# Kernel tuning notes

Measured on AMD Instinct MI355X. Metric: run time of the kernel, lower is better.

## Reference

```python
import jax, jax.numpy as jnp
import numpy as np

N, E_FULL, E_G = 20000, 640000, 160000
IN_DIM, OUT_DIM, H, EDGE_DIM = 128, 16, 8, 128
HD = OUT_DIM * H
SCALE = float(np.sqrt(OUT_DIM))


def setup_inputs() -> dict:
    key = jax.random.key(0)
    ks = jax.random.split(key, 16)

    def lin(k, fi, fo):
        return jax.random.normal(k, (fi, fo), jnp.float32) / np.float32(np.sqrt(fi))

    return {
        "h": jax.random.normal(ks[0], (N, IN_DIM), jnp.float32),
        "e": jax.random.normal(ks[1], (E_G, EDGE_DIM), jnp.float32),
        "adj2": jax.random.uniform(ks[2], (E_FULL, 1), jnp.float32),
        "rel_pos_3d": jax.random.normal(ks[3], (E_FULL, 1), jnp.float32),
        "src": jax.random.randint(ks[4], (E_FULL,), 0, N),
        "dst": jax.random.randint(ks[5], (E_FULL,), 0, N),
        "edge_map": jnp.arange(E_G),  # g's edges are a (unique) subset of full_g's edges
        "Wq": lin(ks[6], IN_DIM, HD), "bq": jnp.zeros((HD,), jnp.float32),
        "Wk": lin(ks[7], IN_DIM, HD), "bk": jnp.zeros((HD,), jnp.float32),
        "Wv": lin(ks[8], IN_DIM, HD), "bv": jnp.zeros((HD,), jnp.float32),
        "Wpe": lin(ks[9], EDGE_DIM, H), "bpe": jnp.zeros((H,), jnp.float32),
        "Wap": lin(ks[10], H, EDGE_DIM), "bap": jnp.zeros((EDGE_DIM,), jnp.float32),
        "Wout": lin(ks[11], HD, HD), "bout": jnp.zeros((HD,), jnp.float32),
        "Woute": lin(ks[12], EDGE_DIM, EDGE_DIM), "boute": jnp.zeros((EDGE_DIM,), jnp.float32),
    }


def reference(h, e, adj2, rel_pos_3d, src, dst, edge_map,
              Wq, bq, Wk, bk, Wv, bv, Wpe, bpe, Wap, bap,
              Wout, bout, Woute, boute):
    Qh = (h @ Wq + bq).reshape(N, H, OUT_DIM)
    Kh = (h @ Wk + bk).reshape(N, H, OUT_DIM)
    Vh = (h @ Wv + bv).reshape(N, H, OUT_DIM)
    proj_e = e @ Wpe + bpe                                       # [E_g, H]

    # full_g edge pipeline: src_dot_dst -> scaling -> dot_exp
    dot = jnp.einsum('ehd,ehd->eh', Kh[src], Qh[dst]) / SCALE    # [E_full, H]
    score = jnp.exp(jnp.clip(dot, -5.0, 5.0) * adj2) + rel_pos_3d  # [E_full, H]

    # extract g's scores, fuse edge features, scatter back
    g_score = score[edge_map]                                    # [E_g, H]
    e_out = g_score @ Wap + bap                                  # attn_proj, [E_g, edge_dim]
    g_score = jnp.clip(g_score, -5.0, 5.0) + proj_e              # imp_exp_attn
    score = score.at[edge_map].set(g_score)                      # partUpdataScore
    score = jnp.exp(jnp.clip(score, -5.0, 5.0))                  # exp

    # send_and_recv: weighted-sum aggregation over full_g edges
    wV = jax.ops.segment_sum(Vh[src] * score[:, :, None], dst, num_segments=N)  # [N, H, D]
    z = jax.ops.segment_sum(score, dst, num_segments=N)                          # [N, H]

    h_out = (wV / (z[:, :, None] + 1e-6)).reshape(N, HD) @ Wout + bout
    e_out = (e_out + e) @ Woute + boute
    return h_out, e_out
```

## Files before the change

kernel.cpp:

```cpp
#include <hip/hip_runtime.h>
#include <hip/hip_bf16.h>

#define NN 20000
#define EF 640000
#define EG 160000
#define SCAN_B 79

typedef __attribute__((ext_vector_type(8))) short bf16x8;
typedef __attribute__((ext_vector_type(4))) float f32x4;
typedef __attribute__((ext_vector_type(2))) float f32x2;

__device__ inline short f2bf(float f) {
    union { float f; unsigned u; } x; x.f = f;
    unsigned r = x.u + 0x7FFF + ((x.u >> 16) & 1);
    return (short)(r >> 16);
}
__device__ inline float bf2f(short s) {
    union { float f; unsigned u; } x;
    x.u = ((unsigned)(unsigned short)s) << 16;
    return x.f;
}
__device__ inline float blo(unsigned u) {
    union { float f; unsigned u; } c; c.u = u << 16; return c.f;
}
__device__ inline float bhi(unsigned u) {
    union { float f; unsigned u; } c; c.u = u & 0xFFFF0000u; return c.f;
}
__device__ inline unsigned pk2(float a, float b) {
    return (unsigned)(unsigned short)f2bf(a) | ((unsigned)(unsigned short)f2bf(b) << 16);
}
__device__ inline float clip5(float v) { return fminf(fmaxf(v, -5.f), 5.f); }

__global__ __launch_bounds__(256) void prep_kernel(
    int* __restrict__ hist, int* __restrict__ inv,
    const float* __restrict__ W0, const float* __restrict__ W1,
    const float* __restrict__ W2, const float* __restrict__ W3,
    const float* __restrict__ W4, short* __restrict__ B0,
    short* __restrict__ B1, short* __restrict__ B2,
    short* __restrict__ B3, short* __restrict__ B4,
    const float* __restrict__ Wpe, short* __restrict__ WpeF,
    const float* __restrict__ Wap, const float* __restrict__ bap,
    const float* __restrict__ Woute, const float* __restrict__ boute,
    short* __restrict__ WcombF, float* __restrict__ bcomb)
{
    int b = blockIdx.x;
    int tid = threadIdx.x;
    if (b < 2500) {
        int i = b * 256 + tid;
        if (i < NN) hist[i] = 0;
        if (i < EF) inv[i] = -1;
    } else if (b < 2540) {
        int u = b - 2500;
        int mat = u >> 3, blk = u & 7;
        const float* W; short* B;
        switch (mat) {
            case 0: W = W0; B = B0; break;
            case 1: W = W1; B = B1; break;
            case 2: W = W2; B = B2; break;
            case 3: W = W3; B = B3; break;
            default: W = W4; B = B4; break;
        }
        int i = blk * 256 + tid;
        int f = i >> 6, lane = i & 63;
        int n = f >> 2, ks = f & 3;
        int col = n * 16 + (lane & 15);
        int k0 = ks * 32 + (lane >> 4) * 8;
        #pragma unroll
        for (int j = 0; j < 8; ++j)
            B[(size_t)i * 8 + j] = f2bf(W[(size_t)(k0 + j) * 128 + col]);
    } else if (b == 2540) {
        int i = tid;
        int lane = i & 63;
        int ks = i >> 6;
        int l15 = lane & 15, lhi = lane >> 4;
        #pragma unroll
        for (int j = 0; j < 8; ++j) {
            int k = ks * 32 + lhi * 8 + j;
            WpeF[(size_t)i * 8 + j] = (l15 < 8) ? f2bf(Wpe[k * 8 + l15]) : 0;
        }
    } else {
        int j = tid;
        if (j < 128) {
            #pragma unroll
            for (int t = 0; t < 32; ++t) WcombF[j * 32 + t] = 0;
        }
        __syncthreads();
        if (j < 128) {
            float bc = boute[j];
            for (int k = 0; k < 128; ++k) bc += bap[k] * Woute[k * 128 + j];
            bcomb[j] = bc;
            int n = j >> 4, l15 = j & 15;
            #pragma unroll
            for (int i = 0; i < 8; ++i) {
                float s = 0.f;
                for (int k = 0; k < 128; ++k) s += Wap[i * 128 + k] * Woute[k * 128 + j];
                WcombF[((size_t)n * 64 + l15) * 8 + i] = f2bf(s);
            }
        }
    }
}

__global__ __launch_bounds__(256) void histinv_kernel(
    const int* __restrict__ dst, int* __restrict__ hist,
    const int* __restrict__ emap, int* __restrict__ inv)
{
    int i = blockIdx.x * 256 + threadIdx.x;
    if (i < EF) atomicAdd(&hist[dst[i]], 1);
    if (i < EG) inv[emap[i]] = i;
}

__global__ __launch_bounds__(256, 2) void qkv_fused(
    const float* __restrict__ h,
    const short* __restrict__ WqF, const short* __restrict__ WkF,
    const short* __restrict__ WvF,
    const float* __restrict__ bq, const float* __restrict__ bk,
    const float* __restrict__ bv,
    short* __restrict__ Qb, short* __restrict__ Kb,
    unsigned char* __restrict__ K8, unsigned char* __restrict__ V8)
{
    int lane = threadIdx.x & 63;
    int w = threadIdx.x >> 6;
    int l15 = lane & 15, lhi = lane >> 4;

    #pragma unroll
    for (int sel = 0; sel < 3; ++sel) {
        const short* BF  = sel == 0 ? WqF : sel == 1 ? WkF : WvF;
        const float* bias = sel == 0 ? bq : sel == 1 ? bk : bv;
        bf16x8 bf[8][4];
        #pragma unroll
        for (int n = 0; n < 8; ++n)
            #pragma unroll
            for (int ks = 0; ks < 4; ++ks)
                bf[n][ks] = *(const bf16x8*)(BF + ((size_t)((n * 4 + ks) * 64 + lane)) * 8);

        for (int t = blockIdx.x; t < 313; t += gridDim.x) {
            int r = t * 64 + w * 16 + l15;
            bool ok = r < NN;
            bf16x8 a[4];
            #pragma unroll
            for (int ks = 0; ks < 4; ++ks) {
                if (ok) {
                    const float* ap = h + (size_t)r * 128 + ks * 32 + lhi * 8;
                    float4 f0 = *(const float4*)ap;
                    float4 f1 = *(const float4*)(ap + 4);
                    a[ks][0] = f2bf(f0.x); a[ks][1] = f2bf(f0.y);
                    a[ks][2] = f2bf(f0.z); a[ks][3] = f2bf(f0.w);
                    a[ks][4] = f2bf(f1.x); a[ks][5] = f2bf(f1.y);
                    a[ks][6] = f2bf(f1.z); a[ks][7] = f2bf(f1.w);
                } else {
                    #pragma unroll
                    for (int j = 0; j < 8; ++j) a[ks][j] = 0;
                }
            }
            #pragma unroll
            for (int n = 0; n < 8; ++n) {
                f32x4 acc = (f32x4){0.f, 0.f, 0.f, 0.f};
                #pragma unroll
                for (int ks = 0; ks < 4; ++ks)
                    acc = __builtin_amdgcn_mfma_f32_16x16x32_bf16(bf[n][ks], a[ks], acc, 0, 0, 0);
                if (!ok) continue;
                int col0 = n * 16 + lhi * 4;
                float4 bs = *(const float4*)(bias + col0);
                float g0 = acc[0] + bs.x, g1 = acc[1] + bs.y;
                float g2 = acc[2] + bs.z, g3 = acc[3] + bs.w;
                if (sel == 0) {
                    *(uint2*)(Qb + (size_t)r * 128 + col0) =
                        make_uint2(pk2(g0, g1), pk2(g2, g3));
                } else if (sel == 1) {
                    *(uint2*)(Kb + (size_t)r * 128 + col0) =
                        make_uint2(pk2(g0, g1), pk2(g2, g3));
                    int w8 = __builtin_amdgcn_cvt_pk_fp8_f32(g0, g1, 0, false);
                    w8 = __builtin_amdgcn_cvt_pk_fp8_f32(g2, g3, w8, true);
                    *(unsigned*)(K8 + (size_t)r * 128 + col0) = (unsigned)w8;
                } else {
                    int w8 = __builtin_amdgcn_cvt_pk_fp8_f32(g0, g1, 0, false);
                    w8 = __builtin_amdgcn_cvt_pk_fp8_f32(g2, g3, w8, true);
                    *(unsigned*)(V8 + (size_t)r * 128 + col0) = (unsigned)w8;
                }
            }
        }
    }
}

__global__ __launch_bounds__(256, 2) void mfma_gemm_abf16(
    const short* __restrict__ Ap, const short* __restrict__ BF,
    const float* __restrict__ bias, float* __restrict__ out, int M)
{
    int lane = threadIdx.x & 63;
    int w = threadIdx.x >> 6;
    int l15 = lane & 15, lhi = lane >> 4;

    bf16x8 bf[8][4];
    #pragma unroll
    for (int n = 0; n < 8; ++n)
        #pragma unroll
        for (int ks = 0; ks < 4; ++ks)
            bf[n][ks] = *(const bf16x8*)(BF + ((size_t)((n * 4 + ks) * 64 + lane)) * 8);

    int ntile = (M + 63) / 64;
    for (int t = blockIdx.x; t < ntile; t += gridDim.x) {
        int r = t * 64 + w * 16 + l15;
        bool ok = r < M;
        bf16x8 a[4];
        #pragma unroll
        for (int ks = 0; ks < 4; ++ks) {
            if (ok) a[ks] = *(const bf16x8*)(Ap + (size_t)r * 128 + ks * 32 + lhi * 8);
            else {
                #pragma unroll
                for (int j = 0; j < 8; ++j) a[ks][j] = 0;
            }
        }
        #pragma unroll
        for (int n = 0; n < 8; ++n) {
            f32x4 acc = (f32x4){0.f, 0.f, 0.f, 0.f};
            #pragma unroll
            for (int ks = 0; ks < 4; ++ks)
                acc = __builtin_amdgcn_mfma_f32_16x16x32_bf16(bf[n][ks], a[ks], acc, 0, 0, 0);
            if (!ok) continue;
            int col0 = n * 16 + lhi * 4;
            float4 bs = *(const float4*)(bias + col0);
            *(float4*)(out + (size_t)r * 128 + col0) =
                make_float4(acc[0] + bs.x, acc[1] + bs.y, acc[2] + bs.z, acc[3] + bs.w);
        }
    }
}

__global__ __launch_bounds__(256) void score_g_kernel(
    const short* __restrict__ Qb, const short* __restrict__ Kb,
    const int* __restrict__ src, const int* __restrict__ dst,
    const float* __restrict__ adj2, const float* __restrict__ rel,
    const int* __restrict__ emap,
    short* __restrict__ gsb, float* __restrict__ s1f)
{
    int tid = blockIdx.x * 256 + threadIdx.x;
    if (tid >= EG * 8) return;
    int i = tid >> 3, hh = tid & 7;
    int e = emap[i];
    int s = src[e], d = dst[e];
    const bf16x8* Kp = (const bf16x8*)(Kb + (size_t)s * 128 + hh * 16);
    const bf16x8* Qp = (const bf16x8*)(Qb + (size_t)d * 128 + hh * 16);
    bf16x8 k0 = Kp[0], k1 = Kp[1];
    bf16x8 q0 = Qp[0], q1 = Qp[1];
    float dot = 0.f;
    #pragma unroll
    for (int j = 0; j < 8; ++j) dot += bf2f(k0[j]) * bf2f(q0[j]);
    #pragma unroll
    for (int j = 0; j < 8; ++j) dot += bf2f(k1[j]) * bf2f(q1[j]);
    dot *= 0.25f;
    float s1 = __expf(clip5(dot) * adj2[e]) + rel[e];
    gsb[tid] = f2bf(s1);
    s1f[tid] = s1;
}

__global__ __launch_bounds__(256, 3) void mfma_eout_pe(
    const float* __restrict__ Ap, const short* __restrict__ WouteF,
    const short* __restrict__ WcombF, const float* __restrict__ bcomb,
    const short* __restrict__ gsb, const short* __restrict__ WpeF,
    const float* __restrict__ bpe, const float* __restrict__ s1f,
    float* __restrict__ out, float* __restrict__ scoreg)
{
    __shared__ short ldsW[16384];
    int tid = threadIdx.x;
    #pragma unroll
    for (int i = 0; i < 8; ++i)
        ((uint4*)ldsW)[tid + i * 256] = ((const uint4*)WouteF)[tid + i * 256];

    int lane = tid & 63;
    int w = tid >> 6;
    int l15 = lane & 15, lhi = lane >> 4;
    int r = blockIdx.x * 64 + w * 16 + l15;

    bf16x8 bc8[8], bp[4];
    #pragma unroll
    for (int n = 0; n < 8; ++n)
        bc8[n] = *(const bf16x8*)(WcombF + ((size_t)(n * 64 + lane)) * 8);
    #pragma unroll
    for (int ks = 0; ks < 4; ++ks)
        bp[ks] = *(const bf16x8*)(WpeF + ((size_t)(ks * 64 + lane)) * 8);

    bf16x8 a[4], ag;
    #pragma unroll
    for (int ks = 0; ks < 4; ++ks) {
        const float* ap = Ap + (size_t)r * 128 + ks * 32 + lhi * 8;
        float4 f0 = *(const float4*)ap;
        float4 f1 = *(const float4*)(ap + 4);
        a[ks][0] = f2bf(f0.x); a[ks][1] = f2bf(f0.y);
        a[ks][2] = f2bf(f0.z); a[ks][3] = f2bf(f0.w);
        a[ks][4] = f2bf(f1.x); a[ks][5] = f2bf(f1.y);
        a[ks][6] = f2bf(f1.z); a[ks][7] = f2bf(f1.w);
    }
    if (lhi == 0) ag = *(const bf16x8*)(gsb + (size_t)r * 8);
    else {
        #pragma unroll
        for (int j = 0; j < 8; ++j) ag[j] = 0;
    }
    __syncthreads();

    #pragma unroll
    for (int n = 0; n < 8; ++n) {
        f32x4 acc = (f32x4){0.f, 0.f, 0.f, 0.f};
        #pragma unroll
        for (int ks = 0; ks < 4; ++ks) {
            bf16x8 b = *(const bf16x8*)(ldsW + ((n * 4 + ks) * 64 + lane) * 8);
            acc = __builtin_amdgcn_mfma_f32_16x16x32_bf16(b, a[ks], acc, 0, 0, 0);
        }
        acc = __builtin_amdgcn_mfma_f32_16x16x32_bf16(bc8[n], ag, acc, 0, 0, 0);
        int col0 = n * 16 + lhi * 4;
        float4 bs = *(const float4*)(bcomb + col0);
        *(float4*)(out + (size_t)r * 128 + col0) =
            make_float4(acc[0] + bs.x, acc[1] + bs.y, acc[2] + bs.z, acc[3] + bs.w);
    }

    f32x4 pacc = (f32x4){0.f, 0.f, 0.f, 0.f};
    #pragma unroll
    for (int ks = 0; ks < 4; ++ks)
        pacc = __builtin_amdgcn_mfma_f32_16x16x32_bf16(bp[ks], a[ks], pacc, 0, 0, 0);
    if (lhi < 2) {
        float4 bs = *(const float4*)(bpe + lhi * 4);
        float4 s1v = *(const float4*)(s1f + (size_t)r * 8 + lhi * 4);
        float4 sg;
        sg.x = __expf(clip5(clip5(s1v.x) + pacc[0] + bs.x));
        sg.y = __expf(clip5(clip5(s1v.y) + pacc[1] + bs.y));
        sg.z = __expf(clip5(clip5(s1v.z) + pacc[2] + bs.z));
        sg.w = __expf(clip5(clip5(s1v.w) + pacc[3] + bs.w));
        *(float4*)(scoreg + (size_t)r * 8 + lhi * 4) = sg;
    }
}

__global__ __launch_bounds__(256) void scan_part(
    const int* __restrict__ hist, int* __restrict__ pref,
    int* __restrict__ bsum)
{
    __shared__ int tmp[256];
    int tid = threadIdx.x;
    int idx = blockIdx.x * 256 + tid;
    int v = (idx < NN) ? hist[idx] : 0;
    tmp[tid] = v;
    __syncthreads();
    for (int s = 1; s < 256; s <<= 1) {
        int t = (tid >= s) ? tmp[tid - s] : 0;
        __syncthreads();
        tmp[tid] += t;
        __syncthreads();
    }
    if (idx < NN) pref[idx] = tmp[tid];
    if (tid == 255) bsum[blockIdx.x] = tmp[255];
}

__global__ __launch_bounds__(128) void scan_bsum(
    const int* __restrict__ bsum, int* __restrict__ bpref)
{
    __shared__ int tmp[128];
    int tid = threadIdx.x;
    int v = (tid < SCAN_B) ? bsum[tid] : 0;
    tmp[tid] = v;
    __syncthreads();
    for (int s = 1; s < 128; s <<= 1) {
        int t = (tid >= s) ? tmp[tid - s] : 0;
        __syncthreads();
        tmp[tid] += t;
        __syncthreads();
    }
    bpref[tid] = tmp[tid] - v;
}

__global__ __launch_bounds__(256) void scan_add(
    const int* __restrict__ pref, const int* __restrict__ bpref,
    const int* __restrict__ hist, int* __restrict__ offs,
    int* __restrict__ cursor)
{
    int idx = blockIdx.x * 256 + threadIdx.x;
    if (idx < NN) {
        int excl = pref[idx] - hist[idx] + bpref[idx >> 8];
        offs[idx] = excl;
        cursor[idx] = excl;
    }
    if (idx == 0) offs[NN] = EF;
}

__global__ __launch_bounds__(256) void scatter_kernel(
    const int* __restrict__ dst, const int* __restrict__ src,
    const int* __restrict__ inv, const float* __restrict__ adj2,
    const float* __restrict__ rel, int* __restrict__ cursor,
    uint2* __restrict__ em)
{
    int i = blockIdx.x * 256 + threadIdx.x;
    if (i < EF) {
        int p = atomicAdd(&cursor[dst[i]], 1);
        int g = inv[i];
        unsigned w0 = (unsigned)src[i] | (g >= 0 ? 0x80000000u : 0u);
        unsigned w1 = (g >= 0) ? (unsigned)g : pk2(adj2[i], rel[i]);
        em[p] = make_uint2(w0, w1);
    }
}

__global__ __launch_bounds__(256) void csr_aggregate_f8(
    const unsigned* __restrict__ Qb2, const unsigned char* __restrict__ K8,
    const unsigned char* __restrict__ V8, const uint2* __restrict__ em,
    const float* __restrict__ scoreg, const int* __restrict__ offs,
    unsigned* __restrict__ wVn)
{
    int lane = threadIdx.x & 63;
    int wid = (blockIdx.x << 2) | (threadIdx.x >> 6);
    if (wid >= NN) return;
    int beg = offs[wid], end = offs[wid + 1];
    int hh = lane >> 3;
    unsigned koff = (unsigned)(lane << 1);

    unsigned qu = Qb2[(unsigned)wid * 64 + lane];
    float qx = blo(qu), qy = bhi(qu);

    float accx = 0.f, accy = 0.f, zacc = 0.f;

#define EB(KW, VW, M)                                                      \
    {                                                                      \
        f32x2 kf = __builtin_amdgcn_cvt_pk_f32_fp8((int)(KW), false);      \
        f32x2 vf = __builtin_amdgcn_cvt_pk_f32_fp8((int)(VW), false);      \
        float px = qx * kf[0] + qy * kf[1];                                \
        px += __shfl_xor(px, 1);                                           \
        px += __shfl_xor(px, 2);                                           \
        px += __shfl_xor(px, 4);                                           \
        bool isg = (int)(M).x < 0;                                         \
        float a2 = blo((M).y), rl = bhi((M).y);                            \
        float t = __expf(clip5(px * 0.25f) * a2) + rl;                     \
        float sc = __expf(clip5(t));                                       \
        unsigned gi = isg ? (M).y : 0u;                                    \
        float sg = scoreg[(size_t)gi * 8 + hh];                            \
        sc = isg ? sg : sc;                                                \
        accx += vf[0] * sc;                                                \
        accy += vf[1] * sc;                                                \
        zacc += sc;                                                        \
    }

    int p = beg;
    for (; p + 4 <= end; p += 4) {
        uint2 m0 = em[p],     m1 = em[p + 1];
        uint2 m2 = em[p + 2], m3 = em[p + 3];
        unsigned s0 = m0.x & 0x7FFFFFFFu, s1 = m1.x & 0x7FFFFFFFu;
        unsigned s2 = m2.x & 0x7FFFFFFFu, s3 = m3.x & 0x7FFFFFFFu;
        unsigned short kw0 = *(const unsigned short*)(K8 + ((s0 << 7) | koff));
        unsigned short kw1 = *(const unsigned short*)(K8 + ((s1 << 7) | koff));
        unsigned short kw2 = *(const unsigned short*)(K8 + ((s2 << 7) | koff));
        unsigned short kw3 = *(const unsigned short*)(K8 + ((s3 << 7) | koff));
        unsigned short vw0 = *(const unsigned short*)(V8 + ((s0 << 7) | koff));
        unsigned short vw1 = *(const unsigned short*)(V8 + ((s1 << 7) | koff));
        unsigned short vw2 = *(const unsigned short*)(V8 + ((s2 << 7) | koff));
        unsigned short vw3 = *(const unsigned short*)(V8 + ((s3 << 7) | koff));
        EB(kw0, vw0, m0)
        EB(kw1, vw1, m1)
        EB(kw2, vw2, m2)
        EB(kw3, vw3, m3)
    }
    for (; p < end; ++p) {
        uint2 m = em[p];
        unsigned s = m.x & 0x7FFFFFFFu;
        unsigned short kw = *(const unsigned short*)(K8 + ((s << 7) | koff));
        unsigned short vw = *(const unsigned short*)(V8 + ((s << 7) | koff));
        EB(kw, vw, m)
    }
#undef EB

    float rz = 1.f / (zacc + 1e-6f);
    unsigned lo = (unsigned short)f2bf(accx * rz);
    unsigned hi = (unsigned short)f2bf(accy * rz);
    wVn[(unsigned)wid * 64 + lane] = lo | (hi << 16);
}

extern "C" void kernel_launch(void* const* d_in, const int* in_sizes, int n_in,
                              void* d_out, int out_size, void* d_ws, size_t ws_size,
                              hipStream_t stream)
{
    const float* h    = (const float*)d_in[0];
    const float* e    = (const float*)d_in[1];
    const float* adj2 = (const float*)d_in[2];
    const float* rel  = (const float*)d_in[3];
    const int*   src  = (const int*)d_in[4];
    const int*   dst  = (const int*)d_in[5];
    const int*   emap = (const int*)d_in[6];
    const float* Wq = (const float*)d_in[7];   const float* bq = (const float*)d_in[8];
    const float* Wk = (const float*)d_in[9];   const float* bk = (const float*)d_in[10];
    const float* Wv = (const float*)d_in[11];  const float* bv = (const float*)d_in[12];
    const float* Wpe = (const float*)d_in[13]; const float* bpe = (const float*)d_in[14];
    const float* Wap = (const float*)d_in[15]; const float* bap = (const float*)d_in[16];
    const float* Wout = (const float*)d_in[17]; const float* bout = (const float*)d_in[18];
    const float* Woute = (const float*)d_in[19]; const float* boute = (const float*)d_in[20];

    float* ws = (float*)d_ws;
    float*    scoreg = ws;
    float*    s1f    = ws + 1280000;
    unsigned* wVn    = (unsigned*)(ws + 2560000);
    short*    Qb     = (short*)(ws + 3840000);
    short*    Kb     = (short*)(ws + 5120000);
    short*    gsb    = (short*)(ws + 6400000);
    unsigned char* K8 = (unsigned char*)(ws + 7040000);
    unsigned char* V8 = (unsigned char*)(ws + 7680000);
    short*    WqF    = (short*)(ws + 8320000);
    short*    WkF    = (short*)(ws + 8328192);
    short*    WvF    = (short*)(ws + 8336384);
    short*    WoutF  = (short*)(ws + 8344576);
    short*    WouteF = (short*)(ws + 8352768);
    short*    WcombF = (short*)(ws + 8360960);
    short*    WpeF   = (short*)(ws + 8363008);
    float*    bcomb  = ws + 8364032;
    uint2*    em     = (uint2*)(ws + 8364160);
    int*      inv    = (int*)(ws + 10924160);
    int*      hist   = (int*)(ws + 11564160);
    int*      offs   = (int*)(ws + 11584160);
    int*      cursor = (int*)(ws + 11604161);
    int*      pref   = (int*)(ws + 11624161);
    int*      bsum   = (int*)(ws + 11644161);
    int*      bpref  = (int*)(ws + 11644289);
    float* h_out = (float*)d_out;
    float* e_out = (float*)d_out + 2560000;

    prep_kernel<<<2542, 256, 0, stream>>>(
        hist, inv, Wq, Wk, Wv, Wout, Woute, WqF, WkF, WvF, WoutF, WouteF,
        Wpe, WpeF, Wap, bap, Woute, boute, WcombF, bcomb);

    histinv_kernel<<<2500, 256, 0, stream>>>(dst, hist, emap, inv);
    scan_part<<<SCAN_B, 256, 0, stream>>>(hist, pref, bsum);
    scan_bsum<<<1, 128, 0, stream>>>(bsum, bpref);
    scan_add<<<SCAN_B, 256, 0, stream>>>(pref, bpref, hist, offs, cursor);
    scatter_kernel<<<2500, 256, 0, stream>>>(dst, src, inv, adj2, rel, cursor, em);

    qkv_fused<<<256, 256, 0, stream>>>(h, WqF, WkF, WvF, bq, bk, bv, Qb, Kb, K8, V8);
    score_g_kernel<<<5000, 256, 0, stream>>>(Qb, Kb, src, dst, adj2, rel, emap,
                                             gsb, s1f);
    mfma_eout_pe<<<2500, 256, 0, stream>>>(e, WouteF, WcombF, bcomb, gsb,
                                           WpeF, bpe, s1f, e_out, scoreg);

    csr_aggregate_f8<<<5000, 256, 0, stream>>>(
        (const unsigned*)Qb, K8, V8, em, scoreg, offs, wVn);

    mfma_gemm_abf16<<<256, 256, 0, stream>>>((const short*)wVn, WoutF, bout, h_out, NN);
}
```

Measured before the change: 227.9 us.

## Merge independent preprocessing kernels into combined launches via block-index partitioning

Independent stages are packed into shared launches by branching on block index. Histogram with QKV, edge scoring with per-block scan, and CSR scatter with e_out/proj_e each share one launch. The separate block-sum scan kernel is removed, and scan_add now reduces the preceding block sums itself. This cuts the launch count from 10 to 6 and lets independent work overlap, at the cost of mixed block types that may hurt occupancy (launch bounds change, LDS reserved for scatter blocks). The scatter write `em[i-(i-p)]` still equals em[p].

```diff
diff --git a/kernel.cpp b/kernel.cpp
--- a/kernel.cpp
+++ b/kernel.cpp
@@ -100,16 +100,9 @@
     }
 }
 
-__global__ __launch_bounds__(256) void histinv_kernel(
+__global__ __launch_bounds__(256, 2) void hq_kernel(
     const int* __restrict__ dst, int* __restrict__ hist,
-    const int* __restrict__ emap, int* __restrict__ inv)
-{
-    int i = blockIdx.x * 256 + threadIdx.x;
-    if (i < EF) atomicAdd(&hist[dst[i]], 1);
-    if (i < EG) inv[emap[i]] = i;
-}
-
-__global__ __launch_bounds__(256, 2) void qkv_fused(
+    const int* __restrict__ emap, int* __restrict__ inv,
     const float* __restrict__ h,
     const short* __restrict__ WqF, const short* __restrict__ WkF,
     const short* __restrict__ WvF,
@@ -118,6 +111,13 @@
     short* __restrict__ Qb, short* __restrict__ Kb,
     unsigned char* __restrict__ K8, unsigned char* __restrict__ V8)
 {
+    if (blockIdx.x < 2500) {
+        int i = blockIdx.x * 256 + threadIdx.x;
+        if (i < EF) atomicAdd(&hist[dst[i]], 1);
+        if (i < EG) inv[emap[i]] = i;
+        return;
+    }
+    int bq0 = blockIdx.x - 2500;
     int lane = threadIdx.x & 63;
     int w = threadIdx.x >> 6;
     int l15 = lane & 15, lhi = lane >> 4;
@@ -133,7 +133,7 @@
             for (int ks = 0; ks < 4; ++ks)
                 bf[n][ks] = *(const bf16x8*)(BF + ((size_t)((n * 4 + ks) * 64 + lane)) * 8);
 
-        for (int t = blockIdx.x; t < 313; t += gridDim.x) {
+        for (int t = bq0; t < 313; t += 256) {
             int r = t * 64 + w * 16 + l15;
             bool ok = r < NN;
             bf16x8 a[4];
@@ -182,77 +182,82 @@
     }
 }
 
-__global__ __launch_bounds__(256, 2) void mfma_gemm_abf16(
-    const short* __restrict__ Ap, const short* __restrict__ BF,
-    const float* __restrict__ bias, float* __restrict__ out, int M)
-{
-    int lane = threadIdx.x & 63;
-    int w = threadIdx.x >> 6;
-    int l15 = lane & 15, lhi = lane >> 4;
-
-    bf16x8 bf[8][4];
-    #pragma unroll
-    for (int n = 0; n < 8; ++n)
-        #pragma unroll
-        for (int ks = 0; ks < 4; ++ks)
-            bf[n][ks] = *(const bf16x8*)(BF + ((size_t)((n * 4 + ks) * 64 + lane)) * 8);
-
-    int ntile = (M + 63) / 64;
-    for (int t = blockIdx.x; t < ntile; t += gridDim.x) {
-        int r = t * 64 + w * 16 + l15;
-        bool ok = r < M;
-        bf16x8 a[4];
-        #pragma unroll
-        for (int ks = 0; ks < 4; ++ks) {
-            if (ok) a[ks] = *(const bf16x8*)(Ap + (size_t)r * 128 + ks * 32 + lhi * 8);
-            else {
-                #pragma unroll
-                for (int j = 0; j < 8; ++j) a[ks][j] = 0;
-            }
-        }
-        #pragma unroll
-        for (int n = 0; n < 8; ++n) {
-            f32x4 acc = (f32x4){0.f, 0.f, 0.f, 0.f};
-            #pragma unroll
-            for (int ks = 0; ks < 4; ++ks)
-                acc = __builtin_amdgcn_mfma_f32_16x16x32_bf16(bf[n][ks], a[ks], acc, 0, 0, 0);
-            if (!ok) continue;
-            int col0 = n * 16 + lhi * 4;
-            float4 bs = *(const float4*)(bias + col0);
-            *(float4*)(out + (size_t)r * 128 + col0) =
-                make_float4(acc[0] + bs.x, acc[1] + bs.y, acc[2] + bs.z, acc[3] + bs.w);
-        }
-    }
-}
-
-__global__ __launch_bounds__(256) void score_g_kernel(
+__global__ __launch_bounds__(256) void sgp_kernel(
     const short* __restrict__ Qb, const short* __restrict__ Kb,
     const int* __restrict__ src, const int* __restrict__ dst,
     const float* __restrict__ adj2, const float* __restrict__ rel,
     const int* __restrict__ emap,
-    short* __restrict__ gsb, float* __restrict__ s1f)
-{
-    int tid = blockIdx.x * 256 + threadIdx.x;
-    if (tid >= EG * 8) return;
-    int i = tid >> 3, hh = tid & 7;
-    int e = emap[i];
-    int s = src[e], d = dst[e];
-    const bf16x8* Kp = (const bf16x8*)(Kb + (size_t)s * 128 + hh * 16);
-    const bf16x8* Qp = (const bf16x8*)(Qb + (size_t)d * 128 + hh * 16);
-    bf16x8 k0 = Kp[0], k1 = Kp[1];
-    bf16x8 q0 = Qp[0], q1 = Qp[1];
-    float dot = 0.f;
-    #pragma unroll
-    for (int j = 0; j < 8; ++j) dot += bf2f(k0[j]) * bf2f(q0[j]);
-    #pragma unroll
-    for (int j = 0; j < 8; ++j) dot += bf2f(k1[j]) * bf2f(q1[j]);
-    dot *= 0.25f;
-    float s1 = __expf(clip5(dot) * adj2[e]) + rel[e];
-    gsb[tid] = f2bf(s1);
-    s1f[tid] = s1;
-}
-
-__global__ __launch_bounds__(256, 3) void mfma_eout_pe(
+    short* __restrict__ gsb, float* __restrict__ s1f,
+    const int* __restrict__ hist, int* __restrict__ pref,
+    int* __restrict__ bsum)
+{
+    __shared__ int tmp[256];
+    if (blockIdx.x < 5000) {
+        int tid = blockIdx.x * 256 + threadIdx.x;
+        if (tid >= EG * 8) return;
+        int i = tid >> 3, hh = tid & 7;
+        int e = emap[i];
+        int s = src[e], d = dst[e];
+        const bf16x8* Kp = (const bf16x8*)(Kb + (size_t)s * 128 + hh * 16);
+        const bf16x8* Qp = (const bf16x8*)(Qb + (size_t)d * 128 + hh * 16);
+        bf16x8 k0 = Kp[0], k1 = Kp[1];
+        bf16x8 q0 = Qp[0], q1 = Qp[1];
+        float dot = 0.f;
+        #pragma unroll
+        for (int j = 0; j < 8; ++j) dot += bf2f(k0[j]) * bf2f(q0[j]);
+        #pragma unroll
+        for (int j = 0; j < 8; ++j) dot += bf2f(k1[j]) * bf2f(q1[j]);
+        dot *= 0.25f;
+        float s1 = __expf(clip5(dot) * adj2[e]) + rel[e];
+        gsb[tid] = f2bf(s1);
+        s1f[tid] = s1;
+        return;
+    }
+    int b = blockIdx.x - 5000;
+    int tid = threadIdx.x;
+    int idx = b * 256 + tid;
+    int v = (idx < NN) ? hist[idx] : 0;
+    tmp[tid] = v;
+    __syncthreads();
+    for (int s = 1; s < 256; s <<= 1) {
+        int t = (tid >= s) ? tmp[tid - s] : 0;
+        __syncthreads();
+        tmp[tid] += t;
+        __syncthreads();
+    }
+    if (idx < NN) pref[idx] = tmp[tid];
+    if (tid == 255) bsum[b] = tmp[255];
+}
+
+__global__ __launch_bounds__(256) void scan_add(
+    const int* __restrict__ pref, const int* __restrict__ bsum,
+    const int* __restrict__ hist, int* __restrict__ offs,
+    int* __restrict__ cursor)
+{
+    __shared__ int red[256];
+    int tid = threadIdx.x;
+    int b = blockIdx.x;
+    red[tid] = (tid < b) ? bsum[tid] : 0;
+    __syncthreads();
+    for (int s = 128; s >= 1; s >>= 1) {
+        if (tid < s) red[tid] += red[tid + s];
+        __syncthreads();
+    }
+    int bp = red[0];
+    int idx = b * 256 + tid;
+    if (idx < NN) {
+        int excl = pref[idx] - hist[idx] + bp;
+        offs[idx] = excl;
+        cursor[idx] = excl;
+    }
+    if (idx == 0) offs[NN] = EF;
+}
+
+__global__ __launch_bounds__(256, 3) void sce_kernel(
+    const int* __restrict__ dst, const int* __restrict__ src,
+    const int* __restrict__ inv, const float* __restrict__ adj2,
+    const float* __restrict__ rel, int* __restrict__ cursor,
+    uint2* __restrict__ em,
     const float* __restrict__ Ap, const short* __restrict__ WouteF,
     const short* __restrict__ WcombF, const float* __restrict__ bcomb,
     const short* __restrict__ gsb, const short* __restrict__ WpeF,
@@ -260,6 +265,18 @@
     float* __restrict__ out, float* __restrict__ scoreg)
 {
     __shared__ short ldsW[16384];
+    if (blockIdx.x < 2500) {
+        int i = blockIdx.x * 256 + threadIdx.x;
+        if (i < EF) {
+            int p = atomicAdd(&cursor[dst[i]], 1);
+            int g = inv[i];
+            unsigned w0 = (unsigned)src[i] | (g >= 0 ? 0x80000000u : 0u);
+            unsigned w1 = (g >= 0) ? (unsigned)g : pk2(adj2[i], rel[i]);
+            em[i - (i - p)] = make_uint2(w0, w1);
+        }
+        return;
+    }
+    int eb = blockIdx.x - 2500;
     int tid = threadIdx.x;
     #pragma unroll
     for (int i = 0; i < 8; ++i)
@@ -268,7 +285,7 @@
     int lane = tid & 63;
     int w = tid >> 6;
     int l15 = lane & 15, lhi = lane >> 4;
-    int r = blockIdx.x * 64 + w * 16 + l15;
+    int r = eb * 64 + w * 16 + l15;
 
     bf16x8 bc8[8], bp[4];
     #pragma unroll
@@ -324,73 +341,6 @@
         sg.z = __expf(clip5(clip5(s1v.z) + pacc[2] + bs.z));
         sg.w = __expf(clip5(clip5(s1v.w) + pacc[3] + bs.w));
         *(float4*)(scoreg + (size_t)r * 8 + lhi * 4) = sg;
-    }
-}
-
-__global__ __launch_bounds__(256) void scan_part(
-    const int* __restrict__ hist, int* __restrict__ pref,
-    int* __restrict__ bsum)
-{
-    __shared__ int tmp[256];
-    int tid = threadIdx.x;
-    int idx = blockIdx.x * 256 + tid;
-    int v = (idx < NN) ? hist[idx] : 0;
-    tmp[tid] = v;
-    __syncthreads();
-    for (int s = 1; s < 256; s <<= 1) {
-        int t = (tid >= s) ? tmp[tid - s] : 0;
-        __syncthreads();
-        tmp[tid] += t;
-        __syncthreads();
-    }
-    if (idx < NN) pref[idx] = tmp[tid];
-    if (tid == 255) bsum[blockIdx.x] = tmp[255];
-}
-
-__global__ __launch_bounds__(128) void scan_bsum(
-    const int* __restrict__ bsum, int* __restrict__ bpref)
-{
-    __shared__ int tmp[128];
-    int tid = threadIdx.x;
-    int v = (tid < SCAN_B) ? bsum[tid] : 0;
-    tmp[tid] = v;
-    __syncthreads();
-    for (int s = 1; s < 128; s <<= 1) {
-        int t = (tid >= s) ? tmp[tid - s] : 0;
-        __syncthreads();
-        tmp[tid] += t;
-        __syncthreads();
-    }
-    bpref[tid] = tmp[tid] - v;
-}
-
-__global__ __launch_bounds__(256) void scan_add(
-    const int* __restrict__ pref, const int* __restrict__ bpref,
-    const int* __restrict__ hist, int* __restrict__ offs,
-    int* __restrict__ cursor)
-{
-    int idx = blockIdx.x * 256 + threadIdx.x;
-    if (idx < NN) {
-        int excl = pref[idx] - hist[idx] + bpref[idx >> 8];
-        offs[idx] = excl;
-        cursor[idx] = excl;
-    }
-    if (idx == 0) offs[NN] = EF;
-}
-
-__global__ __launch_bounds__(256) void scatter_kernel(
-    const int* __restrict__ dst, const int* __restrict__ src,
-    const int* __restrict__ inv, const float* __restrict__ adj2,
-    const float* __restrict__ rel, int* __restrict__ cursor,
-    uint2* __restrict__ em)
-{
-    int i = blockIdx.x * 256 + threadIdx.x;
-    if (i < EF) {
-        int p = atomicAdd(&cursor[dst[i]], 1);
-        int g = inv[i];
-        unsigned w0 = (unsigned)src[i] | (g >= 0 ? 0x80000000u : 0u);
-        unsigned w1 = (g >= 0) ? (unsigned)g : pk2(adj2[i], rel[i]);
-        em[p] = make_uint2(w0, w1);
     }
 }
 
@@ -464,6 +414,49 @@
     unsigned lo = (unsigned short)f2bf(accx * rz);
     unsigned hi = (unsigned short)f2bf(accy * rz);
     wVn[(unsigned)wid * 64 + lane] = lo | (hi << 16);
+}
+
+__global__ __launch_bounds__(256, 2) void mfma_gemm_abf16(
+    const short* __restrict__ Ap, const short* __restrict__ BF,
+    const float* __restrict__ bias, float* __restrict__ out, int M)
+{
+    int lane = threadIdx.x & 63;
+    int w = threadIdx.x >> 6;
+    int l15 = lane & 15, lhi = lane >> 4;
+
+    bf16x8 bf[8][4];
+    #pragma unroll
+    for (int n = 0; n < 8; ++n)
+        #pragma unroll
+        for (int ks = 0; ks < 4; ++ks)
+            bf[n][ks] = *(const bf16x8*)(BF + ((size_t)((n * 4 + ks) * 64 + lane)) * 8);
+
+    int ntile = (M + 63) / 64;
+    for (int t = blockIdx.x; t < ntile; t += gridDim.x) {
+        int r = t * 64 + w * 16 + l15;
+        bool ok = r < M;
+        bf16x8 a[4];
+        #pragma unroll
+        for (int ks = 0; ks < 4; ++ks) {
+            if (ok) a[ks] = *(const bf16x8*)(Ap + (size_t)r * 128 + ks * 32 + lhi * 8);
+            else {
+                #pragma unroll
+                for (int j = 0; j < 8; ++j) a[ks][j] = 0;
+            }
+        }
+        #pragma unroll
+        for (int n = 0; n < 8; ++n) {
+            f32x4 acc = (f32x4){0.f, 0.f, 0.f, 0.f};
+            #pragma unroll
+            for (int ks = 0; ks < 4; ++ks)
+                acc = __builtin_amdgcn_mfma_f32_16x16x32_bf16(bf[n][ks], a[ks], acc, 0, 0, 0);
+            if (!ok) continue;
+            int col0 = n * 16 + lhi * 4;
+            float4 bs = *(const float4*)(bias + col0);
+            *(float4*)(out + (size_t)r * 128 + col0) =
+                make_float4(acc[0] + bs.x, acc[1] + bs.y, acc[2] + bs.z, acc[3] + bs.w);
+        }
+    }
 }
 
 extern "C" void kernel_launch(void* const* d_in, const int* in_sizes, int n_in,
@@ -509,7 +502,6 @@
     int*      cursor = (int*)(ws + 11604161);
     int*      pref   = (int*)(ws + 11624161);
     int*      bsum   = (int*)(ws + 11644161);
-    int*      bpref  = (int*)(ws + 11644289);
     float* h_out = (float*)d_out;
     float* e_out = (float*)d_out + 2560000;
 
@@ -517,17 +509,17 @@
         hist, inv, Wq, Wk, Wv, Wout, Woute, WqF, WkF, WvF, WoutF, WouteF,
         Wpe, WpeF, Wap, bap, Woute, boute, WcombF, bcomb);
 
-    histinv_kernel<<<2500, 256, 0, stream>>>(dst, hist, emap, inv);
-    scan_part<<<SCAN_B, 256, 0, stream>>>(hist, pref, bsum);
-    scan_bsum<<<1, 128, 0, stream>>>(bsum, bpref);
-    scan_add<<<SCAN_B, 256, 0, stream>>>(pref, bpref, hist, offs, cursor);
-    scatter_kernel<<<2500, 256, 0, stream>>>(dst, src, inv, adj2, rel, cursor, em);
-
-    qkv_fused<<<256, 256, 0, stream>>>(h, WqF, WkF, WvF, bq, bk, bv, Qb, Kb, K8, V8);
-    score_g_kernel<<<5000, 256, 0, stream>>>(Qb, Kb, src, dst, adj2, rel, emap,
-                                             gsb, s1f);
-    mfma_eout_pe<<<2500, 256, 0, stream>>>(e, WouteF, WcombF, bcomb, gsb,
-                                           WpeF, bpe, s1f, e_out, scoreg);
+    hq_kernel<<<2756, 256, 0, stream>>>(
+        dst, hist, emap, inv, h, WqF, WkF, WvF, bq, bk, bv, Qb, Kb, K8, V8);
+
+    sgp_kernel<<<5079, 256, 0, stream>>>(
+        Qb, Kb, src, dst, adj2, rel, emap, gsb, s1f, hist, pref, bsum);
+
+    scan_add<<<SCAN_B, 256, 0, stream>>>(pref, bsum, hist, offs, cursor);
+
+    sce_kernel<<<5000, 256, 0, stream>>>(
+        dst, src, inv, adj2, rel, cursor, em,
+        e, WouteF, WcombF, bcomb, gsb, WpeF, bpe, s1f, e_out, scoreg);
 
     csr_aggregate_f8<<<5000, 256, 0, stream>>>(
         (const unsigned*)Qb, K8, V8, em, scoreg, offs, wVn);
```

After: 218.0 us. 1.05x faster.
